# Kernel optimization log

Measured on AMD Instinct MI355X. Metric: run time of the kernel, lower is better.

Reference implementation:

```python
import jax, jax.numpy as jnp
import numpy as np

B, G, C, H = 32, 512, 384, 768
TAU = 0.1
ITERS = 10


def _xavier(key, shape):
    fan_in, fan_out = shape
    lim = (6.0 / (fan_in + fan_out)) ** 0.5
    return jax.random.uniform(key, shape, minval=-lim, maxval=lim, dtype=jnp.float32)


def setup_inputs() -> dict:
    key = jax.random.key(0)
    ks = jax.random.split(key, 4)
    return {
        "center_coords": jax.random.normal(ks[0], (B, G, 3), dtype=jnp.float32),
        "group_features": jax.random.normal(ks[1], (B, G, C), dtype=jnp.float32),
        "W1": _xavier(ks[2], (C, H)),
        "b1": jnp.zeros((H,), jnp.float32),
        "W2": _xavier(ks[3], (H, G)),
        "b2": jnp.zeros((G,), jnp.float32),
    }


def _sinkhorn(scores):
    # scores: (B, G, G); log-space Sinkhorn row/col normalization
    log_alpha = scores / TAU
    for _ in range(ITERS):
        log_alpha = log_alpha - jax.nn.logsumexp(log_alpha, axis=-1, keepdims=True)
        log_alpha = log_alpha - jax.nn.logsumexp(log_alpha, axis=-2, keepdims=True)
    return jnp.exp(log_alpha)


def _greedy_assign(P):
    # Equivalent to torch loop: process entries in descending value order,
    # assign (row, col) if both free == repeatedly take global argmax over
    # entries with free row and free col. P: (G, G) -> perm: (G,) int32.
    g = P.shape[-1]
    flat = P.reshape(-1)

    def step(_, carry):
        row_free, col_free, assign = carry
        mask = (row_free[:, None] & col_free[None, :]).reshape(-1)
        idx = jnp.argmax(jnp.where(mask, flat, -jnp.inf))
        r = idx // g
        c = idx % g
        return (row_free.at[r].set(False), col_free.at[c].set(False), assign.at[r].set(c.astype(jnp.int32)))

    init = (jnp.ones((g,), bool), jnp.ones((g,), bool), jnp.full((g,), -1, jnp.int32))
    _, _, assign = jax.lax.fori_loop(0, g, step, init)
    return assign


def _apply_perm(data, perm):
    # reordered[new_pos] = data[orig_pos]; perm[orig_pos] = new_pos
    return jnp.zeros_like(data).at[perm].set(data)


def reference(center_coords, group_features, W1, b1, W2, b2):
    h = jax.nn.relu(jnp.einsum('bgc,ch->bgh', group_features, W1) + b1)
    scores = jnp.einsum('bgh,hk->bgk', h, W2) + b2  # (B, G, G)
    P = _sinkhorn(scores)
    perm_indices = jax.vmap(_greedy_assign)(P)  # (B, G)
    reordered_coords = jax.vmap(_apply_perm)(center_coords, perm_indices)
    reordered_feats = jax.vmap(_apply_perm)(group_features, perm_indices)
    return reordered_coords, reordered_feats, perm_indices
```

## Files before the change

kernel.cpp:

```cpp
#include <hip/hip_runtime.h>
#include <math.h>

#define NB 32
#define NG 512
#define NC 384
#define NH 768

typedef float f32x4v __attribute__((ext_vector_type(4)));
typedef __bf16 bf16_t;
typedef bf16_t bf16x8 __attribute__((ext_vector_type(8)));
typedef bf16_t bf16x4 __attribute__((ext_vector_type(4)));

__device__ __forceinline__ void split3(float x, bf16_t& h, bf16_t& m, bf16_t& lo)
{
    h = (bf16_t)x;
    float r1 = x - (float)h;
    m = (bf16_t)r1;
    float r2 = r1 - (float)m;
    lo = (bf16_t)r2;
}

__global__ __launch_bounds__(256) void presplit_W(
    const float* __restrict__ W, bf16_t* __restrict__ planeB, int K, int N)
{
    int tid = blockIdx.x * 256 + threadIdx.x;
    int nkc = K >> 5;
    if (tid >= nkc * N) return;
    int kc = tid / N;
    int col = tid - kc * N;
    bf16x8 rh[4], rm[4], rl[4];
#pragma unroll
    for (int k = 0; k < 32; k++) {
        float x = W[(size_t)(kc * 32 + k) * N + col];
        bf16_t h, m, lo;
        split3(x, h, m, lo);
        const int s = (k >> 2) & 3;
        const int sub = ((k >> 4) << 2) + (k & 3);
        rh[s][sub] = h; rm[s][sub] = m; rl[s][sub] = lo;
    }
    int swz = (col >> 1) & 3;
    size_t b0 = ((size_t)(kc * 3 + 0) * N + col) * 32;
    size_t b1 = ((size_t)(kc * 3 + 1) * N + col) * 32;
    size_t b2 = ((size_t)(kc * 3 + 2) * N + col) * 32;
#pragma unroll
    for (int s = 0; s < 4; s++) {
        int d = (s ^ swz) << 3;
        *(bf16x8*)&planeB[b0 + d] = rh[s];
        *(bf16x8*)&planeB[b1 + d] = rm[s];
        *(bf16x8*)&planeB[b2 + d] = rl[s];
    }
}

__global__ __launch_bounds__(256, 4) void gemm_bias_mfma(
    const float* __restrict__ A, const bf16_t* __restrict__ planeB,
    const float* __restrict__ bias, float* __restrict__ Co,
    int M, int N, int K, int mode)
{
    __shared__ __align__(16) bf16_t sA[3][64][32];
    __shared__ __align__(16) bf16_t sB[3][64][32];
    int ntiles = N >> 6;
    int bm = (blockIdx.x / ntiles) << 6;
    int bn = (blockIdx.x % ntiles) << 6;
    int t = threadIdx.x;
    int l = t & 63, w = t >> 6;
    int wr = (w >> 1) << 5;
    int wc = (w & 1) << 5;
    int fr = l & 15;
    int fq = l >> 4;

    int sa_row = t >> 2;
    int sa_k0 = (t & 3) << 3;
    int qA = (sa_k0 >> 2) & 3;
    int hsel = (sa_k0 & 16) ? 4 : 0;
    int aswz = (sa_row >> 1) & 3;
    int colQ0 = ((qA ^ aswz) << 3) + hsel;
    int colQ1 = (((qA + 1) ^ aswz) << 3) + hsel;
    const float* apBase = A + (size_t)(bm + sa_row) * K + sa_k0;

    int sbc = t >> 2;
    int sbs = (t & 3) << 3;

    f32x4v acc[2][2];
#pragma unroll
    for (int i = 0; i < 2; i++)
#pragma unroll
        for (int j = 0; j < 2; j++) acc[i][j] = (f32x4v)(0.f);

    float4 qa0 = *(const float4*)(apBase);
    float4 qa1 = *(const float4*)(apBase + 4);
    bf16x8 pb0 = *(const bf16x8*)&planeB[((size_t)0 * N + bn + sbc) * 32 + sbs];
    bf16x8 pb1 = *(const bf16x8*)&planeB[((size_t)1 * N + bn + sbc) * 32 + sbs];
    bf16x8 pb2 = *(const bf16x8*)&planeB[((size_t)2 * N + bn + sbc) * 32 + sbs];

    for (int kc = 0; kc < K; kc += 32) {
        int kci = kc >> 5;
        __syncthreads();
        {
            float xs[8] = { qa0.x, qa0.y, qa0.z, qa0.w,
                            qa1.x, qa1.y, qa1.z, qa1.w };
            bf16_t hs[8], ms[8], ls[8];
#pragma unroll
            for (int e = 0; e < 8; e++) split3(xs[e], hs[e], ms[e], ls[e]);
            *(bf16x4*)&sA[0][sa_row][colQ0] = (bf16x4){ hs[0], hs[1], hs[2], hs[3] };
            *(bf16x4*)&sA[0][sa_row][colQ1] = (bf16x4){ hs[4], hs[5], hs[6], hs[7] };
            *(bf16x4*)&sA[1][sa_row][colQ0] = (bf16x4){ ms[0], ms[1], ms[2], ms[3] };
            *(bf16x4*)&sA[1][sa_row][colQ1] = (bf16x4){ ms[4], ms[5], ms[6], ms[7] };
            *(bf16x4*)&sA[2][sa_row][colQ0] = (bf16x4){ ls[0], ls[1], ls[2], ls[3] };
            *(bf16x4*)&sA[2][sa_row][colQ1] = (bf16x4){ ls[4], ls[5], ls[6], ls[7] };
        }
        *(bf16x8*)&sB[0][sbc][sbs] = pb0;
        *(bf16x8*)&sB[1][sbc][sbs] = pb1;
        *(bf16x8*)&sB[2][sbc][sbs] = pb2;
        __syncthreads();
        if (kc + 32 < K) {
            const float* ap = apBase + kc + 32;
            qa0 = *(const float4*)(ap);
            qa1 = *(const float4*)(ap + 4);
            pb0 = *(const bf16x8*)&planeB[((size_t)((kci + 1) * 3 + 0) * N + bn + sbc) * 32 + sbs];
            pb1 = *(const bf16x8*)&planeB[((size_t)((kci + 1) * 3 + 1) * N + bn + sbc) * 32 + sbs];
            pb2 = *(const bf16x8*)&planeB[((size_t)((kci + 1) * 3 + 2) * N + bn + sbc) * 32 + sbs];
        }
        bf16x8 afH[2], afM[2], afL[2], bfH[2], bfM[2], bfL[2];
#pragma unroll
        for (int i = 0; i < 2; i++) {
            int ra = wr + i * 16 + fr;
            int pk = (fq ^ ((ra >> 1) & 3)) << 3;
            afH[i] = *(const bf16x8*)&sA[0][ra][pk];
            afM[i] = *(const bf16x8*)&sA[1][ra][pk];
            afL[i] = *(const bf16x8*)&sA[2][ra][pk];
        }
#pragma unroll
        for (int j = 0; j < 2; j++) {
            int rb = wc + j * 16 + fr;
            int pk = (fq ^ ((rb >> 1) & 3)) << 3;
            bfH[j] = *(const bf16x8*)&sB[0][rb][pk];
            bfM[j] = *(const bf16x8*)&sB[1][rb][pk];
            bfL[j] = *(const bf16x8*)&sB[2][rb][pk];
        }
#pragma unroll
        for (int i = 0; i < 2; i++)
#pragma unroll
            for (int j = 0; j < 2; j++) {
                acc[i][j] = __builtin_amdgcn_mfma_f32_16x16x32_bf16(
                    afH[i], bfH[j], acc[i][j], 0, 0, 0);
                acc[i][j] = __builtin_amdgcn_mfma_f32_16x16x32_bf16(
                    afH[i], bfM[j], acc[i][j], 0, 0, 0);
                acc[i][j] = __builtin_amdgcn_mfma_f32_16x16x32_bf16(
                    afM[i], bfH[j], acc[i][j], 0, 0, 0);
                acc[i][j] = __builtin_amdgcn_mfma_f32_16x16x32_bf16(
                    afM[i], bfM[j], acc[i][j], 0, 0, 0);
                acc[i][j] = __builtin_amdgcn_mfma_f32_16x16x32_bf16(
                    afH[i], bfL[j], acc[i][j], 0, 0, 0);
                acc[i][j] = __builtin_amdgcn_mfma_f32_16x16x32_bf16(
                    afL[i], bfH[j], acc[i][j], 0, 0, 0);
            }
    }

    int orow = fq << 2;
#pragma unroll
    for (int j = 0; j < 2; j++) {
        int colg = bn + wc + j * 16 + fr;
        float bj = bias[colg];
#pragma unroll
        for (int i = 0; i < 2; i++) {
            int rowg = bm + wr + i * 16 + orow;
#pragma unroll
            for (int r = 0; r < 4; r++) {
                float val = acc[i][j][r] + bj;
                val = (mode == 0) ? fmaxf(val, 0.f) : val / 0.1f;
                Co[(size_t)(rowg + r) * N + colg] = val;
            }
        }
    }
}

#define DPP6_MAXF(x)                                                              \
    { int _t;                                                                     \
      _t = __builtin_amdgcn_update_dpp(__float_as_int(x), __float_as_int(x),      \
               0x111, 0xf, 0xf, false); x = fmaxf(x, __int_as_float(_t));         \
      _t = __builtin_amdgcn_update_dpp(__float_as_int(x), __float_as_int(x),      \
               0x112, 0xf, 0xf, false); x = fmaxf(x, __int_as_float(_t));         \
      _t = __builtin_amdgcn_update_dpp(__float_as_int(x), __float_as_int(x),      \
               0x114, 0xf, 0xf, false); x = fmaxf(x, __int_as_float(_t));         \
      _t = __builtin_amdgcn_update_dpp(__float_as_int(x), __float_as_int(x),      \
               0x118, 0xf, 0xf, false); x = fmaxf(x, __int_as_float(_t));         \
      _t = __builtin_amdgcn_update_dpp(__float_as_int(x), __float_as_int(x),      \
               0x142, 0xa, 0xf, false); x = fmaxf(x, __int_as_float(_t));         \
      _t = __builtin_amdgcn_update_dpp(__float_as_int(x), __float_as_int(x),      \
               0x143, 0xc, 0xf, false); x = fmaxf(x, __int_as_float(_t)); }

#define DPP6_ADDF(x)                                                              \
    { int _t;                                                                     \
      _t = __builtin_amdgcn_update_dpp(__float_as_int(x), __float_as_int(x),      \
               0x111, 0xf, 0xf, false); x = x + __int_as_float(_t);               \
      _t = __builtin_amdgcn_update_dpp(__float_as_int(x), __float_as_int(x),      \
               0x112, 0xf, 0xf, false); x = x + __int_as_float(_t);               \
      _t = __builtin_amdgcn_update_dpp(__float_as_int(x), __float_as_int(x),      \
               0x114, 0xf, 0xf, false); x = x + __int_as_float(_t);               \
      _t = __builtin_amdgcn_update_dpp(__float_as_int(x), __float_as_int(x),      \
               0x118, 0xf, 0xf, false); x = x + __int_as_float(_t);               \
      _t = __builtin_amdgcn_update_dpp(__float_as_int(x), __float_as_int(x),      \
               0x142, 0xa, 0xf, false); x = x + __int_as_float(_t);               \
      _t = __builtin_amdgcn_update_dpp(__float_as_int(x), __float_as_int(x),      \
               0x143, 0xc, 0xf, false); x = x + __int_as_float(_t); }

__global__ __launch_bounds__(256) void sinkhorn_iter_fused(
    const float* __restrict__ A0, float* __restrict__ uu,
    const float* __restrict__ vIn, float* __restrict__ vOut,
    const float* __restrict__ psIn, float* __restrict__ psOut, int first)
{
    int blk = blockIdx.x;
    int b = blk >> 3, rc = blk & 7;
    int t = threadIdx.x;
    int l = t & 63, w = t >> 6;
    __shared__ __align__(16) float svv[512];

    if (first) {
        svv[t] = 0.f;
        svv[256 + t] = 0.f;
    } else {
#pragma unroll
        for (int h2 = 0; h2 < 2; h2++) {
            int j = h2 * 256 + t;
            float S = 0.f;
#pragma unroll
            for (int r8 = 0; r8 < 8; r8++) S += psIn[((b << 3) + r8) * NG + j];
            float nv = vIn[(b << 9) + j] - __logf(S);
            svv[j] = nv;
            if (rc == 0) vOut[(b << 9) + j] = nv;
        }
    }
    __syncthreads();

    float4 v0 = *(const float4*)(&svv[4 * l]);
    float4 v1 = *(const float4*)(&svv[256 + 4 * l]);
    int row0 = (rc << 6) + (w << 4);
    const float* base = A0 + ((size_t)((b << 9) + row0) << 9);

    float cs0 = 0.f, cs1 = 0.f, cs2 = 0.f, cs3 = 0.f;
    float cs4 = 0.f, cs5 = 0.f, cs6 = 0.f, cs7 = 0.f;

    for (int rr = 0; rr < 16; ++rr) {
        const float* rowp = base + ((size_t)rr << 9);
        float4 a0 = *(const float4*)(rowp + 4 * l);
        float4 a1 = *(const float4*)(rowp + 256 + 4 * l);
        float x0 = a0.x + v0.x, x1 = a0.y + v0.y;
        float x2 = a0.z + v0.z, x3 = a0.w + v0.w;
        float x4 = a1.x + v1.x, x5 = a1.y + v1.y;
        float x6 = a1.z + v1.z, x7 = a1.w + v1.w;
        float m = fmaxf(fmaxf(fmaxf(x0, x1), fmaxf(x2, x3)),
                        fmaxf(fmaxf(x4, x5), fmaxf(x6, x7)));
        DPP6_MAXF(m)
        int mi = __builtin_amdgcn_readlane(__float_as_int(m), 63);
        m = __int_as_float(mi);
        float e0 = __expf(x0 - m), e1 = __expf(x1 - m);
        float e2 = __expf(x2 - m), e3 = __expf(x3 - m);
        float e4 = __expf(x4 - m), e5 = __expf(x5 - m);
        float e6 = __expf(x6 - m), e7 = __expf(x7 - m);
        float s = ((e0 + e1) + (e2 + e3)) + ((e4 + e5) + (e6 + e7));
        DPP6_ADDF(s)
        int si = __builtin_amdgcn_readlane(__float_as_int(s), 63);
        s = __int_as_float(si);
        float inv = 1.0f / s;
        cs0 += e0 * inv; cs1 += e1 * inv; cs2 += e2 * inv; cs3 += e3 * inv;
        cs4 += e4 * inv; cs5 += e5 * inv; cs6 += e6 * inv; cs7 += e7 * inv;
        if (l == 63) uu[(b << 9) + row0 + rr] = -(m + __logf(s));
    }

    __shared__ float sacc[4][512];
    float4 w0; w0.x = cs0; w0.y = cs1; w0.z = cs2; w0.w = cs3;
    float4 w1; w1.x = cs4; w1.y = cs5; w1.z = cs6; w1.w = cs7;
    *(float4*)&sacc[w][4 * l] = w0;
    *(float4*)&sacc[w][256 + 4 * l] = w1;
    __syncthreads();
    float pA = sacc[0][t] + sacc[1][t] + sacc[2][t] + sacc[3][t];
    float pB = sacc[0][256 + t] + sacc[1][256 + t] + sacc[2][256 + t] + sacc[3][256 + t];
    int o = ((b << 3) + rc) * NG;
    psOut[o + t] = pA;
    psOut[o + 256 + t] = pB;
}

__global__ __launch_bounds__(256) void col_combine_final(
    const float* __restrict__ psIn, const float* __restrict__ vIn,
    float* __restrict__ vOut)
{
    int tid = blockIdx.x * 256 + threadIdx.x;
    int b = tid >> 9, j = tid & 511;
    float S = 0.f;
#pragma unroll
    for (int r8 = 0; r8 < 8; r8++) S += psIn[((b << 3) + r8) * NG + j];
    vOut[tid] = vIn[tid] - __logf(S);
}

__device__ __forceinline__ void masked_row_argmax(
    const float* __restrict__ rowp, int l, unsigned int free8, int rr,
    float& outV, int& outF)
{
    float4 x0 = *(const float4*)(rowp + 8 * l);
    float4 x1 = *(const float4*)(rowp + 8 * l + 4);
    float q0 = (free8 & 1u)   ? x0.x : -1.0f;
    float q1 = (free8 & 2u)   ? x0.y : -1.0f;
    float q2 = (free8 & 4u)   ? x0.z : -1.0f;
    float q3 = (free8 & 8u)   ? x0.w : -1.0f;
    float q4 = (free8 & 16u)  ? x1.x : -1.0f;
    float q5 = (free8 & 32u)  ? x1.y : -1.0f;
    float q6 = (free8 & 64u)  ? x1.z : -1.0f;
    float q7 = (free8 & 128u) ? x1.w : -1.0f;
    float lm = fmaxf(fmaxf(fmaxf(q0, q1), fmaxf(q2, q3)),
                     fmaxf(fmaxf(q4, q5), fmaxf(q6, q7)));
    int sb = (rr << 9) + 8 * l;
    int lf = 0x7FFFFFFF;
    lf = (q7 == lm) ? sb + 7 : lf;
    lf = (q6 == lm) ? sb + 6 : lf;
    lf = (q5 == lm) ? sb + 5 : lf;
    lf = (q4 == lm) ? sb + 4 : lf;
    lf = (q3 == lm) ? sb + 3 : lf;
    lf = (q2 == lm) ? sb + 2 : lf;
    lf = (q1 == lm) ? sb + 1 : lf;
    lf = (q0 == lm) ? sb + 0 : lf;
    float gg = lm;
    DPP6_MAXF(gg)
    int ggi = __builtin_amdgcn_readlane(__float_as_int(gg), 63);
    float g1 = __int_as_float(ggi);
    unsigned long long tb = __ballot(lm == g1);
    int tl = __ffsll(tb) - 1;
    outV = g1;
    outF = __builtin_amdgcn_readlane(lf, tl);
}

__global__ __launch_bounds__(256) void p_rowmax(
    const float* __restrict__ A0, const float* __restrict__ uu,
    const float* __restrict__ vv, float* __restrict__ P,
    int* __restrict__ rbCr, int* __restrict__ rbCc,
    unsigned long long* __restrict__ freeRow,
    unsigned long long* __restrict__ freeCol,
    int* __restrict__ remaining)
{
    if (blockIdx.x == 0) {
        int t = threadIdx.x;
        freeRow[t] = ~0ULL;
        freeCol[t] = ~0ULL;
        if (t < NB) remaining[t] = NG;
    }
    int wrow = blockIdx.x * 4 + (threadIdx.x >> 6);
    int l = threadIdx.x & 63;
    int b = wrow >> 9;
    float ur = uu[wrow];
    const float* vb = vv + (b << 9);
    size_t ro = (size_t)wrow << 9;
    float4 a0 = *(const float4*)(A0 + ro + 8 * l);
    float4 a1 = *(const float4*)(A0 + ro + 8 * l + 4);
    float4 v0 = *(const float4*)(vb + 8 * l);
    float4 v1 = *(const float4*)(vb + 8 * l + 4);
    float p0 = expf(a0.x + ur + v0.x);
    float p1 = expf(a0.y + ur + v0.y);
    float p2 = expf(a0.z + ur + v0.z);
    float p3 = expf(a0.w + ur + v0.w);
    float p4 = expf(a1.x + ur + v1.x);
    float p5 = expf(a1.y + ur + v1.y);
    float p6 = expf(a1.z + ur + v1.z);
    float p7 = expf(a1.w + ur + v1.w);
    float4 o0; o0.x = p0; o0.y = p1; o0.z = p2; o0.w = p3;
    float4 o1; o1.x = p4; o1.y = p5; o1.z = p6; o1.w = p7;
    *(float4*)(P + ro + 8 * l) = o0;
    *(float4*)(P + ro + 8 * l + 4) = o1;
    float mv = fmaxf(fmaxf(fmaxf(p0, p1), fmaxf(p2, p3)),
                     fmaxf(fmaxf(p4, p5), fmaxf(p6, p7)));
    int cb = 8 * l;
    int f = 0x7FFFFFFF;
    f = (p7 == mv) ? cb + 7 : f;
    f = (p6 == mv) ? cb + 6 : f;
    f = (p5 == mv) ? cb + 5 : f;
    f = (p4 == mv) ? cb + 4 : f;
    f = (p3 == mv) ? cb + 3 : f;
    f = (p2 == mv) ? cb + 2 : f;
    f = (p1 == mv) ? cb + 1 : f;
    f = (p0 == mv) ? cb + 0 : f;
    float g = mv;
    DPP6_MAXF(g)
    int gi = __builtin_amdgcn_readlane(__float_as_int(g), 63);
    float gm = __int_as_float(gi);
    unsigned long long tb = __ballot(mv == gm);
    int tl = __ffsll(tb) - 1;
    int bestc = __builtin_amdgcn_readlane(f, tl);
    if (l == 0) { rbCr[wrow] = bestc; rbCc[wrow] = -1; }
}

__global__ __launch_bounds__(512) void mutual_round(
    const float* __restrict__ P, int* __restrict__ rbCr, int* __restrict__ rbCc,
    unsigned long long* __restrict__ freeRow,
    unsigned long long* __restrict__ freeCol,
    int* __restrict__ remaining, int* __restrict__ permInt)
{
    int b = blockIdx.x;
    if (remaining[b] == 0) return;
    int t = threadIdx.x;
    int l = t & 63;
    int w = t >> 6;
    const float* Pb = P + (size_t)b * NG * NG;

    __shared__ unsigned int fr[16], fc[16];
    __shared__ int sRC[NG];
    __shared__ int sCC[NG];
    __shared__ int freeList[NG];
    __shared__ int dirtyRows[NG];
    __shared__ int nFree, nDirtyRow, takeCnt;
    __shared__ int wCnt[8], wOff[8];

    if (t < 8) {
        unsigned long long x = freeRow[b * 8 + t];
        fr[2 * t] = (unsigned)x; fr[2 * t + 1] = (unsigned)(x >> 32);
    } else if (t < 16) {
        int i = t - 8;
        unsigned long long x = freeCol[b * 8 + i];
        fc[2 * i] = (unsigned)x; fc[2 * i + 1] = (unsigned)(x >> 32);
    }
    sRC[t] = rbCr[(b << 9) + t];
    sCC[t] = rbCc[(b << 9) + t];
    if (t == 0) { nDirtyRow = 0; takeCnt = 0; }
    __syncthreads();

    bool isFree = (fr[t >> 5] >> (t & 31)) & 1u;
    unsigned long long bm = __ballot(isFree);
    if (l == 0) wCnt[w] = __popcll(bm);
    if (isFree) {
        int c = sRC[t];
        if (!((fc[c >> 5] >> (c & 31)) & 1u)) {
            int d = atomicAdd(&nDirtyRow, 1);
            dirtyRows[d] = t;
        }
    }
    __syncthreads();
    if (t == 0) {
        int s = 0;
#pragma unroll
        for (int i = 0; i < 8; i++) { wOff[i] = s; s += wCnt[i]; }
        nFree = s;
    }
    __syncthreads();
    if (isFree) {
        int rank = __popcll(bm & ((1ULL << l) - 1ULL));
        freeList[wOff[w] + rank] = t;
    }
    __syncthreads();

    int nd = nDirtyRow;
    for (int d = w; d < nd; d += 8) {
        int r = dirtyRows[d];
        unsigned int free8 = (fc[l >> 2] >> ((l & 3) * 8)) & 0xFFu;
        float nv; int nf;
        masked_row_argmax(Pb + ((size_t)r << 9), l, free8, r, nv, nf);
        if (l == 0) {
            int c = nf & 511;
            sRC[r] = c;
            rbCr[(b << 9) + r] = c;
        }
    }
    __syncthreads();

    bool colFree = (fc[t >> 5] >> (t & 31)) & 1u;
    int cachedR = sCC[t];
    bool colDirty = colFree &&
        (cachedR < 0 || !((fr[cachedR >> 5] >> (cachedR & 31)) & 1u));
    if (colDirty) {
        float best = -1.f; int bestr = 0x7FFFFFFF;
        int nf2 = nFree;
        int i = 0;
        for (; i + 4 <= nf2; i += 4) {
            int r0 = freeList[i], r1 = freeList[i + 1];
            int r2 = freeList[i + 2], r3 = freeList[i + 3];
            float v0 = Pb[((size_t)r0 << 9) + t];
            float v1 = Pb[((size_t)r1 << 9) + t];
            float v2 = Pb[((size_t)r2 << 9) + t];
            float v3 = Pb[((size_t)r3 << 9) + t];
            if (v0 > best) { best = v0; bestr = r0; }
            if (v1 > best) { best = v1; bestr = r1; }
            if (v2 > best) { best = v2; bestr = r2; }
            if (v3 > best) { best = v3; bestr = r3; }
        }
        for (; i < nf2; ++i) {
            int ri = freeList[i];
            float vv2 = Pb[((size_t)ri << 9) + t];
            if (vv2 > best) { best = vv2; bestr = ri; }
        }
        sCC[t] = bestr;
        rbCc[(b << 9) + t] = bestr;
    }
    __syncthreads();

    if (colFree) {
        int r = sCC[t];
        if (r >= 0 && r < NG && sRC[r] == t) {
            permInt[(b << 9) + r] = t;
            atomicAnd(&fr[r >> 5], ~(1u << (r & 31)));
            atomicAnd(&fc[t >> 5], ~(1u << (t & 31)));
            atomicAdd(&takeCnt, 1);
        }
    }
    __syncthreads();
    if (t < 8) {
        freeRow[b * 8 + t] =
            ((unsigned long long)fr[2 * t + 1] << 32) | fr[2 * t];
    } else if (t < 16) {
        int i = t - 8;
        freeCol[b * 8 + i] =
            ((unsigned long long)fc[2 * i + 1] << 32) | fc[2 * i];
    }
    if (t == 0) remaining[b] = remaining[b] - takeCnt;
}

__global__ __launch_bounds__(64) void greedy_cleanup(
    const float* __restrict__ P,
    const unsigned long long* __restrict__ freeRow,
    const unsigned long long* __restrict__ freeCol,
    const int* __restrict__ remaining, int* __restrict__ permInt)
{
    int b = blockIdx.x;
    if (remaining[b] == 0) return;
    int l = threadIdx.x;
    const float* Pb = P + (size_t)b * NG * NG;

    unsigned long long wR = freeRow[b * 8 + (l >> 3)];
    unsigned int myRows = (unsigned int)((wR >> ((l & 7) * 8)) & 0xFF);
    unsigned long long wC = freeCol[b * 8 + (l >> 3)];
    unsigned int free8 = (unsigned int)((wC >> ((l & 7) * 8)) & 0xFF);

    float rv[8]; int rf[8];
#pragma unroll
    for (int k = 0; k < 8; k++) { rv[k] = -1.f; rf[k] = 0x7FFFFFFF; }

    int dmk = (int)myRows;
    unsigned long long act = __ballot(dmk != 0);
    while (act) {
        int src = __ffsll(act) - 1;
        int kk = __ffs(__builtin_amdgcn_readlane(dmk, src)) - 1;
        if (l == src) dmk &= ~(1 << kk);
        int rr = (src << 3) + kk;
        float nv; int nf;
        masked_row_argmax(Pb + ((size_t)rr << 9), l, free8, rr, nv, nf);
        bool upd = (l == src);
        rv[0] = (upd && kk == 0) ? nv : rv[0]; rf[0] = (upd && kk == 0) ? nf : rf[0];
        rv[1] = (upd && kk == 1) ? nv : rv[1]; rf[1] = (upd && kk == 1) ? nf : rf[1];
        rv[2] = (upd && kk == 2) ? nv : rv[2]; rf[2] = (upd && kk == 2) ? nf : rf[2];
        rv[3] = (upd && kk == 3) ? nv : rv[3]; rf[3] = (upd && kk == 3) ? nf : rf[3];
        rv[4] = (upd && kk == 4) ? nv : rv[4]; rf[4] = (upd && kk == 4) ? nf : rf[4];
        rv[5] = (upd && kk == 5) ? nv : rv[5]; rf[5] = (upd && kk == 5) ? nf : rf[5];
        rv[6] = (upd && kk == 6) ? nv : rv[6]; rf[6] = (upd && kk == 6) ? nf : rf[6];
        rv[7] = (upd && kk == 7) ? nv : rv[7]; rf[7] = (upd && kk == 7) ? nf : rf[7];
        act = __ballot(dmk != 0);
    }

    for (int step = 0; step < NG; ++step) {
        float mv = fmaxf(fmaxf(fmaxf(rv[0], rv[1]), fmaxf(rv[2], rv[3])),
                         fmaxf(fmaxf(rv[4], rv[5]), fmaxf(rv[6], rv[7])));
        int f = 0x7FFFFFFF;
        f = (rv[7] == mv) ? rf[7] : f;
        f = (rv[6] == mv) ? rf[6] : f;
        f = (rv[5] == mv) ? rf[5] : f;
        f = (rv[4] == mv) ? rf[4] : f;
        f = (rv[3] == mv) ? rf[3] : f;
        f = (rv[2] == mv) ? rf[2] : f;
        f = (rv[1] == mv) ? rf[1] : f;
        f = (rv[0] == mv) ? rf[0] : f;
        float g = mv;
        DPP6_MAXF(g)
        int gi = __builtin_amdgcn_readlane(__float_as_int(g), 63);
        float gm = __int_as_float(gi);
        if (gm < 0.f) break;
        unsigned long long tb = __ballot(mv == gm);
        int tl = __ffsll(tb) - 1;
        int bestf = __builtin_amdgcn_readlane(f, tl);
        int r = bestf >> 9, c = bestf & 511;
        if (l == 0) permInt[(b << 9) + r] = c;
        if (l == (c >> 3)) free8 &= ~(1u << (c & 7));
        int rl = r - (l << 3);
        int dm2 = 0;
#pragma unroll
        for (int k = 0; k < 8; k++) {
            bool alive = rv[k] >= 0.f;
            bool cm = ((rf[k] ^ c) & 511) == 0;
            bool taken = (rl == k);
            if (taken) rv[k] = -1.f;
            dm2 |= (alive && cm && !taken) ? (1 << k) : 0;
        }
        unsigned long long act2 = __ballot(dm2 != 0);
        while (act2) {
            int src = __ffsll(act2) - 1;
            int kk = __ffs(__builtin_amdgcn_readlane(dm2, src)) - 1;
            if (l == src) dm2 &= ~(1 << kk);
            int rr = (src << 3) + kk;
            float nv; int nf;
            masked_row_argmax(Pb + ((size_t)rr << 9), l, free8, rr, nv, nf);
            bool upd = (l == src);
            rv[0] = (upd && kk == 0) ? nv : rv[0]; rf[0] = (upd && kk == 0) ? nf : rf[0];
            rv[1] = (upd && kk == 1) ? nv : rv[1]; rf[1] = (upd && kk == 1) ? nf : rf[1];
            rv[2] = (upd && kk == 2) ? nv : rv[2]; rf[2] = (upd && kk == 2) ? nf : rf[2];
            rv[3] = (upd && kk == 3) ? nv : rv[3]; rf[3] = (upd && kk == 3) ? nf : rf[3];
            rv[4] = (upd && kk == 4) ? nv : rv[4]; rf[4] = (upd && kk == 4) ? nf : rf[4];
            rv[5] = (upd && kk == 5) ? nv : rv[5]; rf[5] = (upd && kk == 5) ? nf : rf[5];
            rv[6] = (upd && kk == 6) ? nv : rv[6]; rf[6] = (upd && kk == 6) ? nf : rf[6];
            rv[7] = (upd && kk == 7) ? nv : rv[7]; rf[7] = (upd && kk == 7) ? nf : rf[7];
            act2 = __ballot(dm2 != 0);
        }
    }
}

__global__ void scatter_all(const float* __restrict__ coords,
    const float* __restrict__ feats, const int* __restrict__ perm,
    float* __restrict__ dstCoords, float* __restrict__ dstFeats,
    float* __restrict__ permF)
{
    int tid = blockIdx.x * 256 + threadIdx.x;
    int rc = tid / 96;
    int q = tid - rc * 96;
    int b = rc >> 9;
    int p = perm[rc];
    const float4* s4 = (const float4*)(feats + (size_t)rc * NC);
    float4* d4 = (float4*)(dstFeats + ((size_t)(b << 9) + p) * NC);
    d4[q] = s4[q];
    if (q == 0) {
        permF[rc] = (float)p;
        size_t so = (size_t)rc * 3;
        size_t dd = ((size_t)(b << 9) + p) * 3;
        dstCoords[dd] = coords[so];
        dstCoords[dd + 1] = coords[so + 1];
        dstCoords[dd + 2] = coords[so + 2];
    }
}

extern "C" void kernel_launch(void* const* d_in, const int* in_sizes, int n_in,
                              void* d_out, int out_size, void* d_ws, size_t ws_size,
                              hipStream_t stream)
{
    const float* coords = (const float*)d_in[0];
    const float* feats  = (const float*)d_in[1];
    const float* W1 = (const float*)d_in[2];
    const float* b1 = (const float*)d_in[3];
    const float* W2 = (const float*)d_in[4];
    const float* b2 = (const float*)d_in[5];

    float* out = (float*)d_out;
    float* outCoords = out;
    float* outFeats  = out + (size_t)NB * NG * 3;
    float* outPerm   = out + (size_t)NB * NG * 3 + (size_t)NB * NG * NC;

    float* ws = (float*)d_ws;
    float* h   = ws;
    float* A0  = h + (size_t)NB * NG * NH;
    float* u   = A0 + (size_t)NB * NG * NG;
    float* vA  = u + NB * NG;
    float* ps0 = vA + NB * NG;
    float* ps1 = ps0 + NB * 8 * NG;
    int* rbCr  = (int*)(ps1 + NB * 8 * NG);
    int* rbCc  = rbCr + NB * NG;
    unsigned long long* freeRow = (unsigned long long*)(rbCc + NB * NG);
    unsigned long long* freeCol = freeRow + NB * 8;
    int* remaining = (int*)(freeCol + NB * 8);
    int* permInt   = remaining + 32;
    float* vB  = (float*)(permInt + NB * NG);
    bf16_t* pB1 = (bf16_t*)(vB + NB * NG);
    bf16_t* pB2 = pB1 + 12 * 3 * NH * 32;

    const int M = NB * NG;

    presplit_W<<<dim3((12 * NH + 255) / 256), 256, 0, stream>>>(W1, pB1, NC, NH);
    presplit_W<<<dim3((24 * NG + 255) / 256), 256, 0, stream>>>(W2, pB2, NH, NG);

    gemm_bias_mfma<<<dim3((M / 64) * (NH / 64)), 256, 0, stream>>>(
        feats, pB1, b1, h, M, NH, NC, 0);
    gemm_bias_mfma<<<dim3((M / 64) * (NG / 64)), 256, 0, stream>>>(
        h, pB2, b2, A0, M, NG, NH, 1);

    hipMemsetAsync(vA, 0, (size_t)NB * NG * sizeof(float), stream);

    float* pbuf[2] = { ps0, ps1 };
    for (int i = 1; i <= 10; ++i) {
        const float* vin = (i % 2 == 0) ? vA : vB;
        float* vout      = (i % 2 == 0) ? vB : vA;
        const float* pin = pbuf[i & 1];
        float* pout      = pbuf[(i - 1) & 1];
        sinkhorn_iter_fused<<<dim3(NB * 8), 256, 0, stream>>>(
            A0, u, vin, vout, pin, pout, (i == 1) ? 1 : 0);
    }
    col_combine_final<<<dim3(M / 256), 256, 0, stream>>>(pbuf[1], vB, vA);

    float* P = h;
    p_rowmax<<<dim3(M / 4), 256, 0, stream>>>(A0, u, vA, P, rbCr, rbCc,
                                              freeRow, freeCol, remaining);

    for (int r = 0; r < 6; ++r)
        mutual_round<<<dim3(NB), 512, 0, stream>>>(P, rbCr, rbCc, freeRow,
                                                   freeCol, remaining, permInt);

    greedy_cleanup<<<dim3(NB), 64, 0, stream>>>(P, freeRow, freeCol,
                                                remaining, permInt);

    scatter_all<<<dim3((NB * NG * 96) / 256), 256, 0, stream>>>(
        coords, feats, permInt, outCoords, outFeats, outPerm);
}
```

Baseline: 409.8 us.

## Widen GEMM tile to 64x128 and load presplit B fragments directly from global

Doubles the N tile of the split-bf16 MFMA GEMM so each wave computes a 32x64 output with 8 accumulators. This halves the number of blocks and the redundant A split work per output column. The B operand no longer goes through shared memory: each lane loads its pre-swizzled fragments straight from the presplit global planes, interleaved with the MFMA sequence. This drops the LDS stores and reads for B, but exposes global load latency inside the k-loop without prefetch and raises register pressure.

```diff
diff --git a/kernel.cpp b/kernel.cpp
--- a/kernel.cpp
+++ b/kernel.cpp
@@ -57,14 +57,13 @@
     int M, int N, int K, int mode)
 {
     __shared__ __align__(16) bf16_t sA[3][64][32];
-    __shared__ __align__(16) bf16_t sB[3][64][32];
-    int ntiles = N >> 6;
+    int ntiles = N >> 7;
     int bm = (blockIdx.x / ntiles) << 6;
-    int bn = (blockIdx.x % ntiles) << 6;
+    int bn = (blockIdx.x % ntiles) << 7;
     int t = threadIdx.x;
     int l = t & 63, w = t >> 6;
     int wr = (w >> 1) << 5;
-    int wc = (w & 1) << 5;
+    int wc = (w & 1) << 6;
     int fr = l & 15;
     int fq = l >> 4;
 
@@ -77,20 +76,22 @@
     int colQ1 = (((qA + 1) ^ aswz) << 3) + hsel;
     const float* apBase = A + (size_t)(bm + sa_row) * K + sa_k0;
 
-    int sbc = t >> 2;
-    int sbs = (t & 3) << 3;
-
-    f32x4v acc[2][2];
+    size_t planeStride = (size_t)N << 5;
+    int rb0 = wc + 0 * 16 + fr, rb1 = wc + 1 * 16 + fr;
+    int rb2 = wc + 2 * 16 + fr, rb3 = wc + 3 * 16 + fr;
+    size_t o0 = ((size_t)(bn + rb0) << 5) + ((fq ^ ((rb0 >> 1) & 3)) << 3);
+    size_t o1 = ((size_t)(bn + rb1) << 5) + ((fq ^ ((rb1 >> 1) & 3)) << 3);
+    size_t o2 = ((size_t)(bn + rb2) << 5) + ((fq ^ ((rb2 >> 1) & 3)) << 3);
+    size_t o3 = ((size_t)(bn + rb3) << 5) + ((fq ^ ((rb3 >> 1) & 3)) << 3);
+
+    f32x4v acc[2][4];
 #pragma unroll
     for (int i = 0; i < 2; i++)
 #pragma unroll
-        for (int j = 0; j < 2; j++) acc[i][j] = (f32x4v)(0.f);
+        for (int j = 0; j < 4; j++) acc[i][j] = (f32x4v)(0.f);
 
     float4 qa0 = *(const float4*)(apBase);
     float4 qa1 = *(const float4*)(apBase + 4);
-    bf16x8 pb0 = *(const bf16x8*)&planeB[((size_t)0 * N + bn + sbc) * 32 + sbs];
-    bf16x8 pb1 = *(const bf16x8*)&planeB[((size_t)1 * N + bn + sbc) * 32 + sbs];
-    bf16x8 pb2 = *(const bf16x8*)&planeB[((size_t)2 * N + bn + sbc) * 32 + sbs];
 
     for (int kc = 0; kc < K; kc += 32) {
         int kci = kc >> 5;
@@ -108,19 +109,20 @@
             *(bf16x4*)&sA[2][sa_row][colQ0] = (bf16x4){ ls[0], ls[1], ls[2], ls[3] };
             *(bf16x4*)&sA[2][sa_row][colQ1] = (bf16x4){ ls[4], ls[5], ls[6], ls[7] };
         }
-        *(bf16x8*)&sB[0][sbc][sbs] = pb0;
-        *(bf16x8*)&sB[1][sbc][sbs] = pb1;
-        *(bf16x8*)&sB[2][sbc][sbs] = pb2;
         __syncthreads();
         if (kc + 32 < K) {
             const float* ap = apBase + kc + 32;
             qa0 = *(const float4*)(ap);
             qa1 = *(const float4*)(ap + 4);
-            pb0 = *(const bf16x8*)&planeB[((size_t)((kci + 1) * 3 + 0) * N + bn + sbc) * 32 + sbs];
-            pb1 = *(const bf16x8*)&planeB[((size_t)((kci + 1) * 3 + 1) * N + bn + sbc) * 32 + sbs];
-            pb2 = *(const bf16x8*)&planeB[((size_t)((kci + 1) * 3 + 2) * N + bn + sbc) * 32 + sbs];
-        }
-        bf16x8 afH[2], afM[2], afL[2], bfH[2], bfM[2], bfL[2];
+        }
+        const bf16_t* pb = planeB + (size_t)(kci * 3) * planeStride;
+        bf16x8 b0H = *(const bf16x8*)&pb[o0];
+        bf16x8 b0M = *(const bf16x8*)&pb[planeStride + o0];
+        bf16x8 b0L = *(const bf16x8*)&pb[2 * planeStride + o0];
+        bf16x8 b1H = *(const bf16x8*)&pb[o1];
+        bf16x8 b1M = *(const bf16x8*)&pb[planeStride + o1];
+        bf16x8 b1L = *(const bf16x8*)&pb[2 * planeStride + o1];
+        bf16x8 afH[2], afM[2], afL[2];
 #pragma unroll
         for (int i = 0; i < 2; i++) {
             int ra = wr + i * 16 + fr;
@@ -129,36 +131,39 @@
             afM[i] = *(const bf16x8*)&sA[1][ra][pk];
             afL[i] = *(const bf16x8*)&sA[2][ra][pk];
         }
-#pragma unroll
-        for (int j = 0; j < 2; j++) {
-            int rb = wc + j * 16 + fr;
-            int pk = (fq ^ ((rb >> 1) & 3)) << 3;
-            bfH[j] = *(const bf16x8*)&sB[0][rb][pk];
-            bfM[j] = *(const bf16x8*)&sB[1][rb][pk];
-            bfL[j] = *(const bf16x8*)&sB[2][rb][pk];
-        }
-#pragma unroll
-        for (int i = 0; i < 2; i++)
-#pragma unroll
-            for (int j = 0; j < 2; j++) {
-                acc[i][j] = __builtin_amdgcn_mfma_f32_16x16x32_bf16(
-                    afH[i], bfH[j], acc[i][j], 0, 0, 0);
-                acc[i][j] = __builtin_amdgcn_mfma_f32_16x16x32_bf16(
-                    afH[i], bfM[j], acc[i][j], 0, 0, 0);
-                acc[i][j] = __builtin_amdgcn_mfma_f32_16x16x32_bf16(
-                    afM[i], bfH[j], acc[i][j], 0, 0, 0);
-                acc[i][j] = __builtin_amdgcn_mfma_f32_16x16x32_bf16(
-                    afM[i], bfM[j], acc[i][j], 0, 0, 0);
-                acc[i][j] = __builtin_amdgcn_mfma_f32_16x16x32_bf16(
-                    afH[i], bfL[j], acc[i][j], 0, 0, 0);
-                acc[i][j] = __builtin_amdgcn_mfma_f32_16x16x32_bf16(
-                    afL[i], bfH[j], acc[i][j], 0, 0, 0);
-            }
+#define MFMA6(i, j, BH, BM, BL)                                               \
+        acc[i][j] = __builtin_amdgcn_mfma_f32_16x16x32_bf16(                  \
+            afH[i], BH, acc[i][j], 0, 0, 0);                                  \
+        acc[i][j] = __builtin_amdgcn_mfma_f32_16x16x32_bf16(                  \
+            afH[i], BM, acc[i][j], 0, 0, 0);                                  \
+        acc[i][j] = __builtin_amdgcn_mfma_f32_16x16x32_bf16(                  \
+            afM[i], BH, acc[i][j], 0, 0, 0);                                  \
+        acc[i][j] = __builtin_amdgcn_mfma_f32_16x16x32_bf16(                  \
+            afM[i], BM, acc[i][j], 0, 0, 0);                                  \
+        acc[i][j] = __builtin_amdgcn_mfma_f32_16x16x32_bf16(                  \
+            afH[i], BL, acc[i][j], 0, 0, 0);                                  \
+        acc[i][j] = __builtin_amdgcn_mfma_f32_16x16x32_bf16(                  \
+            afL[i], BH, acc[i][j], 0, 0, 0);
+        bf16x8 b2H = *(const bf16x8*)&pb[o2];
+        bf16x8 b2M = *(const bf16x8*)&pb[planeStride + o2];
+        bf16x8 b2L = *(const bf16x8*)&pb[2 * planeStride + o2];
+        MFMA6(0, 0, b0H, b0M, b0L)
+        MFMA6(1, 0, b0H, b0M, b0L)
+        bf16x8 b3H = *(const bf16x8*)&pb[o3];
+        bf16x8 b3M = *(const bf16x8*)&pb[planeStride + o3];
+        bf16x8 b3L = *(const bf16x8*)&pb[2 * planeStride + o3];
+        MFMA6(0, 1, b1H, b1M, b1L)
+        MFMA6(1, 1, b1H, b1M, b1L)
+        MFMA6(0, 2, b2H, b2M, b2L)
+        MFMA6(1, 2, b2H, b2M, b2L)
+        MFMA6(0, 3, b3H, b3M, b3L)
+        MFMA6(1, 3, b3H, b3M, b3L)
+#undef MFMA6
     }
 
     int orow = fq << 2;
 #pragma unroll
-    for (int j = 0; j < 2; j++) {
+    for (int j = 0; j < 4; j++) {
         int colg = bn + wc + j * 16 + fr;
         float bj = bias[colg];
 #pragma unroll
@@ -666,9 +671,9 @@
     presplit_W<<<dim3((12 * NH + 255) / 256), 256, 0, stream>>>(W1, pB1, NC, NH);
     presplit_W<<<dim3((24 * NG + 255) / 256), 256, 0, stream>>>(W2, pB2, NH, NG);
 
-    gemm_bias_mfma<<<dim3((M / 64) * (NH / 64)), 256, 0, stream>>>(
+    gemm_bias_mfma<<<dim3((M / 64) * (NH / 128)), 256, 0, stream>>>(
         feats, pB1, b1, h, M, NH, NC, 0);
-    gemm_bias_mfma<<<dim3((M / 64) * (NG / 64)), 256, 0, stream>>>(
+    gemm_bias_mfma<<<dim3((M / 64) * (NG / 128)), 256, 0, stream>>>(
         h, pB2, b2, A0, M, NG, NH, 1);
 
     hipMemsetAsync(vA, 0, (size_t)NB * NG * sizeof(float), stream);
```

Result: no change. 403.7 us (-1.5%).
